# Performance work log

Measured on AMD Instinct MI355X. Metric: run time of the kernel, lower is better.

The kernel has to match this reference:

```python
import jax, jax.numpy as jnp
import numpy as np

B, S, D = 2, 2048, 512
E, H, TOP_K = 8, 1024, 2
SCALE = 1.0


def setup_inputs() -> dict:
    key = jax.random.key(0)
    ks = jax.random.split(key, 7)
    s = lambda fan_in: 1.0 / np.sqrt(fan_in)
    return {
        "x": jax.random.normal(ks[0], (B, S, D), dtype=jnp.float32),
        "gate_w": jax.random.normal(ks[1], (E, D), dtype=jnp.float32) * s(D),
        "w1": jax.random.normal(ks[2], (E, H, D), dtype=jnp.float32) * s(D),
        "w2": jax.random.normal(ks[3], (E, D, H), dtype=jnp.float32) * s(H),
        "sg_gate": jax.random.normal(ks[4], (H, D), dtype=jnp.float32) * s(D),
        "sg_up": jax.random.normal(ks[5], (H, D), dtype=jnp.float32) * s(D),
        "sg_down": jax.random.normal(ks[6], (D, H), dtype=jnp.float32) * s(H),
    }


def reference(x, gate_w, w1, w2, sg_gate, sg_up, sg_down):
    b, s_len, d = x.shape
    xf = x.reshape(-1, d)                      # [N, D]
    n = xf.shape[0]

    # --- TopKRouter: logits -> top-k -> softmax over the k selected logits ---
    logits = (xf @ gate_w.T) * SCALE           # [N, E]
    topk_w, idx = jax.lax.top_k(logits, TOP_K)  # [N, K]
    topk_w = jax.nn.softmax(topk_w, axis=-1)
    # per-token combine weights scattered to expert slots: [N, E]
    comb = jnp.zeros((n, E), dtype=xf.dtype).at[jnp.arange(n)[:, None], idx].add(topk_w)

    # --- Routed experts (dense masked compute; weight 0 for unrouted) ---
    h = jax.nn.silu(jnp.einsum('td,ehd->teh', xf, w1))   # [N, E, H]
    eo = jnp.einsum('teh,edh->ted', h, w2)               # [N, E, D]
    routed = jnp.einsum('te,ted->td', comb, eo)          # [N, D]

    # --- Shared expert (SwiGLU), n_shared_experts = 1 ---
    shared = (jax.nn.silu(xf @ sg_gate.T) * (xf @ sg_up.T)) @ sg_down.T

    return (routed + shared).reshape(b, s_len, d)
```

## Files before the change

### kernel.cpp

```cpp
#include <hip/hip_runtime.h>
#include <hip/hip_bf16.h>


#define NTOK 4096
#define DDIM 512
#define HDIM 1024
#define NEXP 8
#define CAP  4096

typedef unsigned short u16;
typedef __attribute__((ext_vector_type(8))) short short8;
typedef __attribute__((ext_vector_type(4))) float f32x4;

__device__ __forceinline__ u16 f2bf(float f) {
  unsigned u = __float_as_uint(f);
  u += 0x7fffu + ((u >> 16) & 1u);
  return (u16)(u >> 16);
}
__device__ __forceinline__ float bf2f(u16 v) {
  return __uint_as_float(((unsigned)v) << 16);
}
__device__ __forceinline__ float silu_f(float v) { return v / (1.0f + __expf(-v)); }

__device__ __forceinline__ void gload16(const u16* g, u16* l) {
  __builtin_amdgcn_global_load_lds((const __attribute__((address_space(1))) void*)g,
                                   (__attribute__((address_space(3))) void*)l, 16, 0, 0);
}

__global__ __launch_bounds__(256) void prep(
    const float* __restrict__ x,   const float* __restrict__ gw,
    const float* __restrict__ w1,  const float* __restrict__ w2,
    const float* __restrict__ sgg, const float* __restrict__ sgu,
    const float* __restrict__ sgd,
    u16* __restrict__ Xb, u16* __restrict__ W1b, u16* __restrict__ W2b,
    u16* __restrict__ SGGb, u16* __restrict__ SGUb, u16* __restrict__ SGDb,
    int* __restrict__ tIdx, float2* __restrict__ tW) {
  if (blockIdx.x < NTOK / 4) {
    const int lane = threadIdx.x & 63;
    const int wid  = threadIdx.x >> 6;
    const int t = blockIdx.x * 4 + wid;
    const float4* xr = (const float4*)(x + (size_t)t * DDIM + lane * 8);
    const float4 x0 = xr[0], x1 = xr[1];
    short8 xbv;
    xbv[0]=f2bf(x0.x); xbv[1]=f2bf(x0.y); xbv[2]=f2bf(x0.z); xbv[3]=f2bf(x0.w);
    xbv[4]=f2bf(x1.x); xbv[5]=f2bf(x1.y); xbv[6]=f2bf(x1.z); xbv[7]=f2bf(x1.w);
    *(short8*)&Xb[(size_t)t * DDIM + lane * 8] = xbv;
    float p[NEXP];
#pragma unroll
    for (int e = 0; e < NEXP; ++e) {
      const float4* gr = (const float4*)(gw + (size_t)e * DDIM + lane * 8);
      const float4 g0 = gr[0], g1 = gr[1];
      p[e] = x0.x*g0.x + x0.y*g0.y + x0.z*g0.z + x0.w*g0.w +
             x1.x*g1.x + x1.y*g1.y + x1.z*g1.z + x1.w*g1.w;
    }
#pragma unroll
    for (int e = 0; e < NEXP; ++e) {
#pragma unroll
      for (int m = 32; m >= 1; m >>= 1) p[e] += __shfl_xor(p[e], m);
    }
    if (lane == 0) {
      int i0 = 0; float v0 = p[0];
#pragma unroll
      for (int e = 1; e < NEXP; ++e) if (p[e] > v0) { v0 = p[e]; i0 = e; }
      int i1 = -1; float v1 = -3.0e38f;
#pragma unroll
      for (int e = 0; e < NEXP; ++e) if (e != i0 && p[e] > v1) { v1 = p[e]; i1 = e; }
      const float ex1 = __expf(v1 - v0);
      const float inv = 1.0f / (1.0f + ex1);
      tIdx[t] = i0 | (i1 << 4);
      tW[t] = make_float2(inv, ex1 * inv);
    }
  } else {
    constexpr int NW1 = NEXP * HDIM * DDIM / 4;
    constexpr int NSG = HDIM * DDIM / 4;
    constexpr int TOT = 2 * NW1 + 3 * NSG;
    int i = (blockIdx.x - NTOK / 4) * 256 + threadIdx.x;
    const int stride = (gridDim.x - NTOK / 4) * 256;
    for (; i < TOT; i += stride) {
      const float* s; u16* d; int j = i;
      if (j < NW1)               { s = w1;  d = W1b;  }
      else if ((j -= NW1) < NW1) { s = w2;  d = W2b;  }
      else if ((j -= NW1) < NSG) { s = sgg; d = SGGb; }
      else if ((j -= NSG) < NSG) { s = sgu; d = SGUb; }
      else        { j -= NSG;      s = sgd; d = SGDb; }
      float4 v = ((const float4*)s)[j];
      ushort4 o;
      o.x = f2bf(v.x); o.y = f2bf(v.y); o.z = f2bf(v.z); o.w = f2bf(v.w);
      ((ushort4*)d)[j] = o;
    }
  }
}

__global__ __launch_bounds__(256) void build_lists(
    const int* __restrict__ tIdx,
    int* __restrict__ counts, int* __restrict__ elist) {
  const int e = blockIdx.x;
  __shared__ int cnt;
  if (threadIdx.x == 0) cnt = 0;
  __syncthreads();
  const int lane = threadIdx.x & 63;
  int* el = elist + e * CAP;
  for (int base = 0; base < NTOK; base += 256) {
    const int t = base + threadIdx.x;
    const int pk = tIdx[t];
#pragma unroll
    for (int slot = 0; slot < 2; ++slot) {
      const bool m = (((pk >> (slot * 4)) & 15) == e);
      const unsigned long long b = __ballot(m);
      const int my  = __popcll(b & ((1ull << lane) - 1));
      const int tot = __popcll(b);
      int wbase = 0;
      if (lane == 0 && tot) wbase = atomicAdd(&cnt, tot);
      wbase = __shfl(wbase, 0);
      if (m) el[wbase + my] = t * 2 + slot;
    }
  }
  __syncthreads();
  if (threadIdx.x == 0) counts[e] = cnt;
}

__global__ __launch_bounds__(256, 4) void gemm_up(
    const u16* __restrict__ Xb, const u16* __restrict__ W1b,
    const u16* __restrict__ SGGb, const u16* __restrict__ SGUb,
    u16* __restrict__ Hbuf, u16* __restrict__ Gtmp, u16* __restrict__ Utmp,
    const int* __restrict__ counts, const int* __restrict__ elist) {
  constexpr int KDIM = DDIM, KSTEP = KDIM / 32;
  const int z = blockIdx.z;
  const int n0 = blockIdx.x * 128;
  const int m0 = blockIdx.y * 128;
  const bool routed = (z < NEXP);

  int mlim; const u16* Bp; const int* lst = nullptr;
  if (routed) {
    mlim = counts[z];
    lst = elist + z * CAP;
    Bp = W1b + (size_t)z * HDIM * KDIM;
  } else {
    mlim = NTOK;
    Bp = (z == NEXP) ? SGGb : SGUb;
  }
  if (m0 >= mlim) return;

  __shared__ __align__(16) u16 As[2][128 * 32];
  __shared__ __align__(16) u16 Bs[2][128 * 32];
  __shared__ int rowE[128];

  const int tid = threadIdx.x;
  const int wid = tid >> 6, lane = tid & 63;

  if (routed) {
    if (tid < 128) {
      int idx = m0 + tid; if (idx > mlim - 1) idx = mlim - 1;
      rowE[tid] = lst[idx];
    }
    __syncthreads();
  }

  const u16 *aG[2], *bG[2];
  u16 *aL[2][2], *bL[2][2];
#pragma unroll
  for (int p = 0; p < 2; ++p) {
    const int slot = (wid + p * 4) * 64 + lane;
    const int r = slot >> 2, kc = slot & 3;
#pragma unroll
    for (int c = 0; c < 2; ++c) {
      aL[c][p] = &As[c][slot * 8];
      bL[c][p] = &Bs[c][slot * 8];
    }
    const int arow = routed ? (rowE[r] >> 1) : (m0 + r);
    aG[p] = Xb + (size_t)arow * KDIM + kc * 8;
    bG[p] = Bp + (size_t)(n0 + r) * KDIM + kc * 8;
  }

  const int wm = (wid >> 1) * 64, wn = (wid & 1) * 64;
  const int lr = lane & 15, lk = lane >> 4;

  const f32x4 zero = {0.f, 0.f, 0.f, 0.f};
  f32x4 acc[4][4];
#pragma unroll
  for (int i = 0; i < 4; ++i)
#pragma unroll
    for (int j = 0; j < 4; ++j) acc[i][j] = zero;

  auto STAGE = [&](int kt, int c) {
#pragma unroll
    for (int p = 0; p < 2; ++p) {
      gload16(aG[p] + kt * 32, aL[c][p]);
      gload16(bG[p] + kt * 32, bL[c][p]);
    }
  };

  STAGE(0, 0);
  STAGE(1, 1);
  int cur = 0;
  for (int kt = 0; kt < KSTEP; ++kt) {
    if (kt + 1 < KSTEP) asm volatile("s_waitcnt vmcnt(4)" ::: "memory");
    else                asm volatile("s_waitcnt vmcnt(0)" ::: "memory");
    __builtin_amdgcn_s_barrier();
    short8 a[4], b[4];
#pragma unroll
    for (int i = 0; i < 4; ++i)
      a[i] = *(const short8*)&As[cur][(wm + i * 16 + lr) * 32 + lk * 8];
#pragma unroll
    for (int j = 0; j < 4; ++j)
      b[j] = *(const short8*)&Bs[cur][(wn + j * 16 + lr) * 32 + lk * 8];
    asm volatile("s_waitcnt lgkmcnt(0)" ::: "memory");
    __builtin_amdgcn_sched_barrier(0);
    __builtin_amdgcn_s_barrier();
    if (kt + 2 < KSTEP) STAGE(kt + 2, cur);
#pragma unroll
    for (int i = 0; i < 4; ++i)
#pragma unroll
      for (int j = 0; j < 4; ++j)
        acc[i][j] = __builtin_amdgcn_mfma_f32_16x16x32_bf16(a[i], b[j], acc[i][j], 0, 0, 0);
    cur ^= 1;
  }

#pragma unroll
  for (int i = 0; i < 4; ++i) {
#pragma unroll
    for (int j = 0; j < 4; ++j) {
      const int col = n0 + wn + j * 16 + lr;
#pragma unroll
      for (int r = 0; r < 4; ++r) {
        const int m = wm + i * 16 + lk * 4 + r;
        if (routed) {
          if (m0 + m < mlim)
            Hbuf[(size_t)rowE[m] * HDIM + col] = f2bf(silu_f(acc[i][j][r]));
        } else if (z == NEXP) {
          Gtmp[(size_t)(m0 + m) * HDIM + col] = f2bf(silu_f(acc[i][j][r]));
        } else {
          Utmp[(size_t)(m0 + m) * HDIM + col] = f2bf(acc[i][j][r]);
        }
      }
    }
  }
}

__global__ __launch_bounds__(256) void fuse_act(
    const u16* __restrict__ G, const u16* __restrict__ U, u16* __restrict__ ACT) {
  const int i = blockIdx.x * 256 + threadIdx.x;
  const short8 g = *(const short8*)&G[(size_t)i * 8];
  const short8 u = *(const short8*)&U[(size_t)i * 8];
  short8 o;
#pragma unroll
  for (int k = 0; k < 8; ++k)
    o[k] = (short)f2bf(bf2f((u16)g[k]) * bf2f((u16)u[k]));
  *(short8*)&ACT[(size_t)i * 8] = o;
}

__global__ __launch_bounds__(256, 4) void gemm_down(
    const u16* __restrict__ Hbuf, const u16* __restrict__ W2b,
    const u16* __restrict__ ACT,  const u16* __restrict__ SGDb,
    u16* __restrict__ eo, float* __restrict__ out,
    const int* __restrict__ counts, const int* __restrict__ elist) {
  constexpr int KDIM = HDIM, KSTEP = KDIM / 32;
  const int z = blockIdx.z;
  const int n0 = blockIdx.x * 128;
  const int m0 = blockIdx.y * 128;
  const bool routed = (z < NEXP);

  int mlim; const u16* Ap; const u16* Bp; const int* lst = nullptr;
  if (routed) {
    mlim = counts[z];
    lst = elist + z * CAP;
    Ap = Hbuf;
    Bp = W2b + (size_t)z * DDIM * KDIM;
  } else {
    mlim = NTOK;
    Ap = ACT;
    Bp = SGDb;
  }
  if (m0 >= mlim) return;

  __shared__ __align__(16) u16 As[2][128 * 32];
  __shared__ __align__(16) u16 Bs[2][128 * 32];
  __shared__ int rowE[128];

  const int tid = threadIdx.x;
  const int wid = tid >> 6, lane = tid & 63;

  if (routed) {
    if (tid < 128) {
      int idx = m0 + tid; if (idx > mlim - 1) idx = mlim - 1;
      rowE[tid] = lst[idx];
    }
    __syncthreads();
  }

  const u16 *aG[2], *bG[2];
  u16 *aL[2][2], *bL[2][2];
#pragma unroll
  for (int p = 0; p < 2; ++p) {
    const int slot = (wid + p * 4) * 64 + lane;
    const int r = slot >> 2, kc = slot & 3;
#pragma unroll
    for (int c = 0; c < 2; ++c) {
      aL[c][p] = &As[c][slot * 8];
      bL[c][p] = &Bs[c][slot * 8];
    }
    const int arow = routed ? rowE[r] : (m0 + r);
    aG[p] = Ap + (size_t)arow * KDIM + kc * 8;
    bG[p] = Bp + (size_t)(n0 + r) * KDIM + kc * 8;
  }

  const int wm = (wid >> 1) * 64, wn = (wid & 1) * 64;
  const int lr = lane & 15, lk = lane >> 4;

  const f32x4 zero = {0.f, 0.f, 0.f, 0.f};
  f32x4 acc[4][4];
#pragma unroll
  for (int i = 0; i < 4; ++i)
#pragma unroll
    for (int j = 0; j < 4; ++j) acc[i][j] = zero;

  auto STAGE = [&](int kt, int c) {
#pragma unroll
    for (int p = 0; p < 2; ++p) {
      gload16(aG[p] + kt * 32, aL[c][p]);
      gload16(bG[p] + kt * 32, bL[c][p]);
    }
  };

  STAGE(0, 0);
  STAGE(1, 1);
  int cur = 0;
  for (int kt = 0; kt < KSTEP; ++kt) {
    if (kt + 1 < KSTEP) asm volatile("s_waitcnt vmcnt(4)" ::: "memory");
    else                asm volatile("s_waitcnt vmcnt(0)" ::: "memory");
    __builtin_amdgcn_s_barrier();
    short8 a[4], b[4];
#pragma unroll
    for (int i = 0; i < 4; ++i)
      a[i] = *(const short8*)&As[cur][(wm + i * 16 + lr) * 32 + lk * 8];
#pragma unroll
    for (int j = 0; j < 4; ++j)
      b[j] = *(const short8*)&Bs[cur][(wn + j * 16 + lr) * 32 + lk * 8];
    asm volatile("s_waitcnt lgkmcnt(0)" ::: "memory");
    __builtin_amdgcn_sched_barrier(0);
    __builtin_amdgcn_s_barrier();
    if (kt + 2 < KSTEP) STAGE(kt + 2, cur);
#pragma unroll
    for (int i = 0; i < 4; ++i)
#pragma unroll
      for (int j = 0; j < 4; ++j)
        acc[i][j] = __builtin_amdgcn_mfma_f32_16x16x32_bf16(a[i], b[j], acc[i][j], 0, 0, 0);
    cur ^= 1;
  }

#pragma unroll
  for (int i = 0; i < 4; ++i) {
#pragma unroll
    for (int j = 0; j < 4; ++j) {
      const int col = n0 + wn + j * 16 + lr;
#pragma unroll
      for (int r = 0; r < 4; ++r) {
        const int m = wm + i * 16 + lk * 4 + r;
        if (routed) {
          if (m0 + m < mlim)
            eo[(size_t)rowE[m] * DDIM + col] = f2bf(acc[i][j][r]);
        } else {
          out[(size_t)(m0 + m) * DDIM + col] = acc[i][j][r];
        }
      }
    }
  }
}

__global__ __launch_bounds__(256) void combine_kernel(
    const u16* __restrict__ eo, const float2* __restrict__ tW,
    float* __restrict__ out) {
  const int g = blockIdx.x * 256 + threadIdx.x;
  const int t = g >> 6;
  const int c0 = (g & 63) * 8;
  const float2 w = tW[t];
  const short8 e0 = *(const short8*)&eo[(size_t)(t * 2) * DDIM + c0];
  const short8 e1 = *(const short8*)&eo[(size_t)(t * 2 + 1) * DDIM + c0];
  float* o = out + (size_t)t * DDIM + c0;
  float4 o0 = ((float4*)o)[0], o1 = ((float4*)o)[1];
  o0.x += w.x * bf2f((u16)e0[0]) + w.y * bf2f((u16)e1[0]);
  o0.y += w.x * bf2f((u16)e0[1]) + w.y * bf2f((u16)e1[1]);
  o0.z += w.x * bf2f((u16)e0[2]) + w.y * bf2f((u16)e1[2]);
  o0.w += w.x * bf2f((u16)e0[3]) + w.y * bf2f((u16)e1[3]);
  o1.x += w.x * bf2f((u16)e0[4]) + w.y * bf2f((u16)e1[4]);
  o1.y += w.x * bf2f((u16)e0[5]) + w.y * bf2f((u16)e1[5]);
  o1.z += w.x * bf2f((u16)e0[6]) + w.y * bf2f((u16)e1[6]);
  o1.w += w.x * bf2f((u16)e0[7]) + w.y * bf2f((u16)e1[7]);
  ((float4*)o)[0] = o0; ((float4*)o)[1] = o1;
}

extern "C" void kernel_launch(void* const* d_in, const int* in_sizes, int n_in,
                              void* d_out, int out_size, void* d_ws, size_t ws_size,
                              hipStream_t stream) {
  const float* x    = (const float*)d_in[0];
  const float* gw   = (const float*)d_in[1];
  const float* w1   = (const float*)d_in[2];
  const float* w2   = (const float*)d_in[3];
  const float* sgg  = (const float*)d_in[4];
  const float* sgu  = (const float*)d_in[5];
  const float* sgd  = (const float*)d_in[6];
  float* out = (float*)d_out;

  char* ws = (char*)d_ws;
  size_t off = 0;
  auto take = [&](size_t bytes) {
    size_t r = off; off += (bytes + 255) & ~(size_t)255; return r;
  };
  int*    counts = (int*)   (ws + take(NEXP * sizeof(int)));
  int*    elist  = (int*)   (ws + take((size_t)NEXP * CAP * sizeof(int)));
  int*    tIdx   = (int*)   (ws + take((size_t)NTOK * sizeof(int)));
  float2* tW     = (float2*)(ws + take((size_t)NTOK * sizeof(float2)));
  u16*    Xb     = (u16*)   (ws + take((size_t)NTOK * DDIM * 2));
  u16*    W1b    = (u16*)   (ws + take((size_t)NEXP * HDIM * DDIM * 2));
  u16*    W2b    = (u16*)   (ws + take((size_t)NEXP * DDIM * HDIM * 2));
  u16*    SGGb   = (u16*)   (ws + take((size_t)HDIM * DDIM * 2));
  u16*    SGUb   = (u16*)   (ws + take((size_t)HDIM * DDIM * 2));
  u16*    SGDb   = (u16*)   (ws + take((size_t)DDIM * HDIM * 2));
  u16*    Hbuf   = (u16*)   (ws + take((size_t)NTOK * 2 * HDIM * 2));
  u16*    ACT    = (u16*)   (ws + take((size_t)NTOK * HDIM * 2));
  u16*    Gtmp   = (u16*)   (ws + take((size_t)NTOK * HDIM * 2));
  u16*    Utmp   = (u16*)   (ws + take((size_t)NTOK * HDIM * 2));
  u16*    eo     = W1b;
  if (off > ws_size) return;

  prep<<<dim3(3072), 256, 0, stream>>>(x, gw, w1, w2, sgg, sgu, sgd,
                                       Xb, W1b, W2b, SGGb, SGUb, SGDb, tIdx, tW);
  build_lists<<<NEXP, 256, 0, stream>>>(tIdx, counts, elist);
  gemm_up<<<dim3(HDIM / 128, 32, NEXP + 2), 256, 0, stream>>>(
      Xb, W1b, SGGb, SGUb, Hbuf, Gtmp, Utmp, counts, elist);
  fuse_act<<<NTOK * HDIM / 8 / 256, 256, 0, stream>>>(Gtmp, Utmp, ACT);
  gemm_down<<<dim3(DDIM / 128, 32, NEXP + 1), 256, 0, stream>>>(
      Hbuf, W2b, ACT, SGDb, eo, out, counts, elist);
  combine_kernel<<<NTOK * 64 / 256, 256, 0, stream>>>(eo, tW, out);
}
```

Baseline: 125.1 us.

## Split-K down GEMM, triple-buffer GEMM pipelines, and swizzle block order across XCDs

The down-projection GEMM now splits K into two halves, which doubles the number of blocks. Each half writes a separate partial buffer, and the combine kernel sums the two. Both GEMMs move from double to triple LDS buffering with deeper vmcnt waits, and occupancy drops to 3 blocks per CU to make room. A block-index swizzle reorders work so that consecutive tiles land on the same XCD, which should improve L2 reuse. The cost is extra partial-buffer traffic and reduced occupancy.

```diff
diff --git a/kernel.cpp b/kernel.cpp
--- a/kernel.cpp
+++ b/kernel.cpp
@@ -25,6 +25,16 @@
 __device__ __forceinline__ void gload16(const u16* g, u16* l) {
   __builtin_amdgcn_global_load_lds((const __attribute__((address_space(1))) void*)g,
                                    (__attribute__((address_space(3))) void*)l, 16, 0, 0);
+}
+
+template <int NX, int NY, int NWG8>
+__device__ __forceinline__ void swz_decode(int& x, int& y, int& z) {
+  const int h = blockIdx.x + gridDim.x * (blockIdx.y + gridDim.y * blockIdx.z);
+  const int work = (h & 7) * NWG8 + (h >> 3);
+  x = work % NX;
+  const int q = work / NX;
+  y = q % NY;
+  z = q / NY;
 }
 
 __global__ __launch_bounds__(256) void prep(
@@ -119,15 +129,16 @@
   if (threadIdx.x == 0) counts[e] = cnt;
 }
 
-__global__ __launch_bounds__(256, 4) void gemm_up(
+__global__ __launch_bounds__(256, 3) void gemm_up(
     const u16* __restrict__ Xb, const u16* __restrict__ W1b,
     const u16* __restrict__ SGGb, const u16* __restrict__ SGUb,
     u16* __restrict__ Hbuf, u16* __restrict__ Gtmp, u16* __restrict__ Utmp,
     const int* __restrict__ counts, const int* __restrict__ elist) {
   constexpr int KDIM = DDIM, KSTEP = KDIM / 32;
-  const int z = blockIdx.z;
-  const int n0 = blockIdx.x * 128;
-  const int m0 = blockIdx.y * 128;
+  int bx, by, z;
+  swz_decode<HDIM / 128, 32, (HDIM / 128) * 32 * (NEXP + 2) / 8>(bx, by, z);
+  const int n0 = bx * 128;
+  const int m0 = by * 128;
   const bool routed = (z < NEXP);
 
   int mlim; const u16* Bp; const int* lst = nullptr;
@@ -141,8 +152,8 @@
   }
   if (m0 >= mlim) return;
 
-  __shared__ __align__(16) u16 As[2][128 * 32];
-  __shared__ __align__(16) u16 Bs[2][128 * 32];
+  __shared__ __align__(16) u16 As[3][128 * 32];
+  __shared__ __align__(16) u16 Bs[3][128 * 32];
   __shared__ int rowE[128];
 
   const int tid = threadIdx.x;
@@ -157,13 +168,13 @@
   }
 
   const u16 *aG[2], *bG[2];
-  u16 *aL[2][2], *bL[2][2];
+  u16 *aL[3][2], *bL[3][2];
 #pragma unroll
   for (int p = 0; p < 2; ++p) {
     const int slot = (wid + p * 4) * 64 + lane;
     const int r = slot >> 2, kc = slot & 3;
 #pragma unroll
-    for (int c = 0; c < 2; ++c) {
+    for (int c = 0; c < 3; ++c) {
       aL[c][p] = &As[c][slot * 8];
       bL[c][p] = &Bs[c][slot * 8];
     }
@@ -190,12 +201,12 @@
     }
   };
 
-  STAGE(0, 0);
-  STAGE(1, 1);
+  STAGE(0, 0); STAGE(1, 1); STAGE(2, 2);
   int cur = 0;
   for (int kt = 0; kt < KSTEP; ++kt) {
-    if (kt + 1 < KSTEP) asm volatile("s_waitcnt vmcnt(4)" ::: "memory");
-    else                asm volatile("s_waitcnt vmcnt(0)" ::: "memory");
+    if (kt + 2 < KSTEP)      asm volatile("s_waitcnt vmcnt(8)" ::: "memory");
+    else if (kt + 1 < KSTEP) asm volatile("s_waitcnt vmcnt(4)" ::: "memory");
+    else                     asm volatile("s_waitcnt vmcnt(0)" ::: "memory");
     __builtin_amdgcn_s_barrier();
     short8 a[4], b[4];
 #pragma unroll
@@ -207,13 +218,13 @@
     asm volatile("s_waitcnt lgkmcnt(0)" ::: "memory");
     __builtin_amdgcn_sched_barrier(0);
     __builtin_amdgcn_s_barrier();
-    if (kt + 2 < KSTEP) STAGE(kt + 2, cur);
+    if (kt + 3 < KSTEP) STAGE(kt + 3, cur);
 #pragma unroll
     for (int i = 0; i < 4; ++i)
 #pragma unroll
       for (int j = 0; j < 4; ++j)
         acc[i][j] = __builtin_amdgcn_mfma_f32_16x16x32_bf16(a[i], b[j], acc[i][j], 0, 0, 0);
-    cur ^= 1;
+    cur = (cur == 2) ? 0 : cur + 1;
   }
 
 #pragma unroll
@@ -249,23 +260,29 @@
   *(short8*)&ACT[(size_t)i * 8] = o;
 }
 
-__global__ __launch_bounds__(256, 4) void gemm_down(
+__global__ __launch_bounds__(256, 3) void gemm_down(
     const u16* __restrict__ Hbuf, const u16* __restrict__ W2b,
     const u16* __restrict__ ACT,  const u16* __restrict__ SGDb,
-    u16* __restrict__ eo, float* __restrict__ out,
+    u16* __restrict__ eo0, u16* __restrict__ eo1,
+    float* __restrict__ sh0, float* __restrict__ sh1,
     const int* __restrict__ counts, const int* __restrict__ elist) {
-  constexpr int KDIM = HDIM, KSTEP = KDIM / 32;
-  const int z = blockIdx.z;
-  const int n0 = blockIdx.x * 128;
-  const int m0 = blockIdx.y * 128;
-  const bool routed = (z < NEXP);
+  constexpr int KFULL = HDIM;
+  constexpr int KSTEP = 512 / 32;
+  int bx, by, z;
+  swz_decode<DDIM / 128, 32, (DDIM / 128) * 32 * (2 * NEXP + 2) / 8>(bx, by, z);
+  const int n0 = bx * 128;
+  const int m0 = by * 128;
+  const bool routed = (z < 2 * NEXP);
+  const int khalf = routed ? (z & 1) : (z - 2 * NEXP);
+  const int koff = khalf * 512;
 
   int mlim; const u16* Ap; const u16* Bp; const int* lst = nullptr;
   if (routed) {
-    mlim = counts[z];
-    lst = elist + z * CAP;
+    const int e = z >> 1;
+    mlim = counts[e];
+    lst = elist + e * CAP;
     Ap = Hbuf;
-    Bp = W2b + (size_t)z * DDIM * KDIM;
+    Bp = W2b + (size_t)e * DDIM * KFULL;
   } else {
     mlim = NTOK;
     Ap = ACT;
@@ -273,8 +290,8 @@
   }
   if (m0 >= mlim) return;
 
-  __shared__ __align__(16) u16 As[2][128 * 32];
-  __shared__ __align__(16) u16 Bs[2][128 * 32];
+  __shared__ __align__(16) u16 As[3][128 * 32];
+  __shared__ __align__(16) u16 Bs[3][128 * 32];
   __shared__ int rowE[128];
 
   const int tid = threadIdx.x;
@@ -289,19 +306,19 @@
   }
 
   const u16 *aG[2], *bG[2];
-  u16 *aL[2][2], *bL[2][2];
+  u16 *aL[3][2], *bL[3][2];
 #pragma unroll
   for (int p = 0; p < 2; ++p) {
     const int slot = (wid + p * 4) * 64 + lane;
     const int r = slot >> 2, kc = slot & 3;
 #pragma unroll
-    for (int c = 0; c < 2; ++c) {
+    for (int c = 0; c < 3; ++c) {
       aL[c][p] = &As[c][slot * 8];
       bL[c][p] = &Bs[c][slot * 8];
     }
     const int arow = routed ? rowE[r] : (m0 + r);
-    aG[p] = Ap + (size_t)arow * KDIM + kc * 8;
-    bG[p] = Bp + (size_t)(n0 + r) * KDIM + kc * 8;
+    aG[p] = Ap + (size_t)arow * KFULL + koff + kc * 8;
+    bG[p] = Bp + (size_t)(n0 + r) * KFULL + koff + kc * 8;
   }
 
   const int wm = (wid >> 1) * 64, wn = (wid & 1) * 64;
@@ -322,12 +339,12 @@
     }
   };
 
-  STAGE(0, 0);
-  STAGE(1, 1);
+  STAGE(0, 0); STAGE(1, 1); STAGE(2, 2);
   int cur = 0;
   for (int kt = 0; kt < KSTEP; ++kt) {
-    if (kt + 1 < KSTEP) asm volatile("s_waitcnt vmcnt(4)" ::: "memory");
-    else                asm volatile("s_waitcnt vmcnt(0)" ::: "memory");
+    if (kt + 2 < KSTEP)      asm volatile("s_waitcnt vmcnt(8)" ::: "memory");
+    else if (kt + 1 < KSTEP) asm volatile("s_waitcnt vmcnt(4)" ::: "memory");
+    else                     asm volatile("s_waitcnt vmcnt(0)" ::: "memory");
     __builtin_amdgcn_s_barrier();
     short8 a[4], b[4];
 #pragma unroll
@@ -339,13 +356,13 @@
     asm volatile("s_waitcnt lgkmcnt(0)" ::: "memory");
     __builtin_amdgcn_sched_barrier(0);
     __builtin_amdgcn_s_barrier();
-    if (kt + 2 < KSTEP) STAGE(kt + 2, cur);
+    if (kt + 3 < KSTEP) STAGE(kt + 3, cur);
 #pragma unroll
     for (int i = 0; i < 4; ++i)
 #pragma unroll
       for (int j = 0; j < 4; ++j)
         acc[i][j] = __builtin_amdgcn_mfma_f32_16x16x32_bf16(a[i], b[j], acc[i][j], 0, 0, 0);
-    cur ^= 1;
+    cur = (cur == 2) ? 0 : cur + 1;
   }
 
 #pragma unroll
@@ -357,10 +374,13 @@
       for (int r = 0; r < 4; ++r) {
         const int m = wm + i * 16 + lk * 4 + r;
         if (routed) {
-          if (m0 + m < mlim)
-            eo[(size_t)rowE[m] * DDIM + col] = f2bf(acc[i][j][r]);
+          if (m0 + m < mlim) {
+            u16* dst = khalf ? eo1 : eo0;
+            dst[(size_t)rowE[m] * DDIM + col] = f2bf(acc[i][j][r]);
+          }
         } else {
-          out[(size_t)(m0 + m) * DDIM + col] = acc[i][j][r];
+          float* dst = khalf ? sh1 : sh0;
+          dst[(size_t)(m0 + m) * DDIM + col] = acc[i][j][r];
         }
       }
     }
@@ -368,25 +388,35 @@
 }
 
 __global__ __launch_bounds__(256) void combine_kernel(
-    const u16* __restrict__ eo, const float2* __restrict__ tW,
-    float* __restrict__ out) {
+    const u16* __restrict__ eo0, const u16* __restrict__ eo1,
+    const float* __restrict__ sh0, const float* __restrict__ sh1,
+    const float2* __restrict__ tW, float* __restrict__ out) {
   const int g = blockIdx.x * 256 + threadIdx.x;
   const int t = g >> 6;
   const int c0 = (g & 63) * 8;
   const float2 w = tW[t];
-  const short8 e0 = *(const short8*)&eo[(size_t)(t * 2) * DDIM + c0];
-  const short8 e1 = *(const short8*)&eo[(size_t)(t * 2 + 1) * DDIM + c0];
-  float* o = out + (size_t)t * DDIM + c0;
-  float4 o0 = ((float4*)o)[0], o1 = ((float4*)o)[1];
-  o0.x += w.x * bf2f((u16)e0[0]) + w.y * bf2f((u16)e1[0]);
-  o0.y += w.x * bf2f((u16)e0[1]) + w.y * bf2f((u16)e1[1]);
-  o0.z += w.x * bf2f((u16)e0[2]) + w.y * bf2f((u16)e1[2]);
-  o0.w += w.x * bf2f((u16)e0[3]) + w.y * bf2f((u16)e1[3]);
-  o1.x += w.x * bf2f((u16)e0[4]) + w.y * bf2f((u16)e1[4]);
-  o1.y += w.x * bf2f((u16)e0[5]) + w.y * bf2f((u16)e1[5]);
-  o1.z += w.x * bf2f((u16)e0[6]) + w.y * bf2f((u16)e1[6]);
-  o1.w += w.x * bf2f((u16)e0[7]) + w.y * bf2f((u16)e1[7]);
-  ((float4*)o)[0] = o0; ((float4*)o)[1] = o1;
+  const size_t r0 = (size_t)(t * 2) * DDIM + c0;
+  const size_t r1 = (size_t)(t * 2 + 1) * DDIM + c0;
+  const short8 a0 = *(const short8*)&eo0[r0];
+  const short8 a1 = *(const short8*)&eo0[r1];
+  const short8 b0 = *(const short8*)&eo1[r0];
+  const short8 b1 = *(const short8*)&eo1[r1];
+  const size_t so = (size_t)t * DDIM + c0;
+  const float4 s0a = ((const float4*)(sh0 + so))[0];
+  const float4 s0b = ((const float4*)(sh0 + so))[1];
+  const float4 s1a = ((const float4*)(sh1 + so))[0];
+  const float4 s1b = ((const float4*)(sh1 + so))[1];
+  float o[8];
+  o[0]=s0a.x+s1a.x; o[1]=s0a.y+s1a.y; o[2]=s0a.z+s1a.z; o[3]=s0a.w+s1a.w;
+  o[4]=s0b.x+s1b.x; o[5]=s0b.y+s1b.y; o[6]=s0b.z+s1b.z; o[7]=s0b.w+s1b.w;
+#pragma unroll
+  for (int k = 0; k < 8; ++k)
+    o[k] += w.x * (bf2f((u16)a0[k]) + bf2f((u16)b0[k])) +
+            w.y * (bf2f((u16)a1[k]) + bf2f((u16)b1[k]));
+  float4 v0 = {o[0], o[1], o[2], o[3]};
+  float4 v1 = {o[4], o[5], o[6], o[7]};
+  ((float4*)(out + so))[0] = v0;
+  ((float4*)(out + so))[1] = v1;
 }
 
 extern "C" void kernel_launch(void* const* d_in, const int* in_sizes, int n_in,
@@ -420,7 +450,10 @@
   u16*    ACT    = (u16*)   (ws + take((size_t)NTOK * HDIM * 2));
   u16*    Gtmp   = (u16*)   (ws + take((size_t)NTOK * HDIM * 2));
   u16*    Utmp   = (u16*)   (ws + take((size_t)NTOK * HDIM * 2));
-  u16*    eo     = W1b;
+  u16*    eo0    = (u16*)   (ws + take((size_t)NTOK * 2 * DDIM * 2));
+  u16*    eo1    = (u16*)   (ws + take((size_t)NTOK * 2 * DDIM * 2));
+  float*  sh0    = (float*) (ws + take((size_t)NTOK * DDIM * 4));
+  float*  sh1    = (float*) (ws + take((size_t)NTOK * DDIM * 4));
   if (off > ws_size) return;
 
   prep<<<dim3(3072), 256, 0, stream>>>(x, gw, w1, w2, sgg, sgu, sgd,
@@ -429,7 +462,7 @@
   gemm_up<<<dim3(HDIM / 128, 32, NEXP + 2), 256, 0, stream>>>(
       Xb, W1b, SGGb, SGUb, Hbuf, Gtmp, Utmp, counts, elist);
   fuse_act<<<NTOK * HDIM / 8 / 256, 256, 0, stream>>>(Gtmp, Utmp, ACT);
-  gemm_down<<<dim3(DDIM / 128, 32, NEXP + 1), 256, 0, stream>>>(
-      Hbuf, W2b, ACT, SGDb, eo, out, counts, elist);
-  combine_kernel<<<NTOK * 64 / 256, 256, 0, stream>>>(eo, tW, out);
-}
+  gemm_down<<<dim3(DDIM / 128, 32, 2 * NEXP + 2), 256, 0, stream>>>(
+      Hbuf, W2b, ACT, SGDb, eo0, eo1, sh0, sh1, counts, elist);
+  combine_kernel<<<NTOK * 64 / 256, 256, 0, stream>>>(eo0, eo1, sh0, sh1, tW, out);
+}
```

Result: slower. 144.3 us (+15.3%).
